# Kernel tuning notes

Measured on AMD Instinct MI355X. Metric: run time of the kernel, lower is better.

Reference implementation:

```python
import jax, jax.numpy as jnp
import numpy as np

LEAKY_ALPHA = 0.2
EPS_NORM = 1e-07


def _leaky_relu(x):
    return jnp.where(x >= 0, x, LEAKY_ALPHA * x)


def setup_inputs() -> dict:
    key = jax.random.key(0)
    ks = jax.random.split(key, 10)
    B, N, F = 16, 1024, 256
    H, Q, K, V = 4, 128, 128, 128
    return {
        "e": jax.random.normal(ks[0], (B, N, N), dtype=jnp.float32),
        "x_atm": jax.random.normal(ks[1], (B, N, F), dtype=jnp.float32),
        "mask": jnp.ones((B, N), dtype=jnp.float32),
        "eps": jax.random.normal(ks[2], (1,), dtype=jnp.float32) * 0.02,
        "Wq": jax.random.normal(ks[3], (H, F, Q), dtype=jnp.float32) * 0.05,
        "Wk": jax.random.normal(ks[4], (H, F, K), dtype=jnp.float32) * 0.05,
        "Wv": jax.random.normal(ks[5], (H, F, V), dtype=jnp.float32) * 0.05,
        "aq": jax.random.normal(ks[6], (H, Q), dtype=jnp.float32) * 0.05,
        "bq": jnp.zeros((H,), dtype=jnp.float32),
        "ak": jax.random.normal(ks[7], (H, K), dtype=jnp.float32) * 0.05,
        "bk": jnp.zeros((H,), dtype=jnp.float32),
    }


def reference(e, x_atm, mask, eps, Wq, Wk, Wv, aq, bq, ak, bk):
    B, N, _ = e.shape
    # add learned eps to the diagonal of e (set_diag(diag + eps))
    e_mod = e + eps[0] * jnp.eye(N, dtype=e.dtype)  # [B,N,N]

    # per-head query/key scalars: Dense -> LeakyReLU -> Dense(1)
    q = jnp.einsum("bhnq,hq->bhn", _leaky_relu(jnp.einsum("bnf,hfq->bhnq", x_atm, Wq)), aq) + bq[None, :, None]  # [B,H,N]
    k = jnp.einsum("bhnk,hk->bhn", _leaky_relu(jnp.einsum("bnf,hfk->bhnk", x_atm, Wk)), ak) + bk[None, :, None]  # [B,H,N]

    # attn[b,h,i,j] = tanh((q_i + k_j) * e_mod[b,i,j])
    scores = jnp.tanh((q[..., :, None] + k[..., None, :]) * e_mod[:, None, :, :])  # [B,H,N,N]

    # L2-normalize each row (tf.linalg.normalize norm + 1e-7)
    norm = jnp.sqrt(jnp.sum(scores * scores, axis=-1, keepdims=True)) + EPS_NORM
    attn = scores / norm

    # values and aggregation
    v = jnp.einsum("bnf,hfv->bhnv", x_atm, Wv)  # [B,H,N,V] (dropout rate 0 -> identity)
    out = jnp.einsum("bhij,bhjv->bhiv", attn, v)  # [B,H,N,V]

    # pooling == 'mask': sum over nodes weighted by mask -> [B,H,V]
    pooled = jnp.einsum("bhnv,bn->bhv", out, mask)

    # concat heads along feature axis -> [B, H*V]
    return pooled.reshape(B, -1)
```

## Files before the change

kernel.cpp:

```cpp
#include <hip/hip_runtime.h>

#define B_ 16
#define N_ 1024
#define F_ 256
#define H_ 4
#define QDIM 128

#define TANH_PRESCALE 2.8853900817779268f

typedef __attribute__((ext_vector_type(8))) short bf16x8;
typedef __attribute__((ext_vector_type(4))) float f32x4;
typedef __attribute__((ext_vector_type(2))) float f32x2;

__device__ __forceinline__ float leaky(float x) {
    return x >= 0.f ? x : 0.2f * x;
}

__device__ __forceinline__ unsigned short bfbits(float f) {
    unsigned u = __float_as_uint(f);
    return (unsigned short)((u + 0x7fffu + ((u >> 16) & 1u)) >> 16);
}

__device__ __forceinline__ float bf2f(unsigned short u) {
    return __uint_as_float(((unsigned)u) << 16);
}

__global__ __launch_bounds__(256) void convert_all(
    const float4* __restrict__ x4, ushort4* __restrict__ xh4,
    const float* __restrict__ Wq, const float* __restrict__ Wk,
    ushort* __restrict__ Wqt, ushort* __restrict__ Wkt)
{
    const int bx = blockIdx.x;
    if (bx < 2048) {
        const int t = bx * 256 + threadIdx.x;
        const float4 a = x4[2 * t], b = x4[2 * t + 1];
        ushort4 o0, o1;
        o0.x = bfbits(a.x); o0.y = bfbits(a.y); o0.z = bfbits(a.z); o0.w = bfbits(a.w);
        o1.x = bfbits(b.x); o1.y = bfbits(b.y); o1.z = bfbits(b.z); o1.w = bfbits(b.w);
        xh4[2 * t] = o0; xh4[2 * t + 1] = o1;
    } else {
        const int t2 = (bx - 2048) * 256 + threadIdx.x;
        const int z = t2 >> 17, t = t2 & 131071;
        const int f = t & 255, q = (t >> 8) & 127, h = t >> 15;
        const float* W = z ? Wk : Wq;
        ushort* O = z ? Wkt : Wqt;
        O[t] = bfbits(W[(h * 256 + f) * 128 + q]);
    }
}

__global__ __launch_bounds__(256) void qk_mfma(
    const ushort* __restrict__ xh,
    const ushort* __restrict__ Wqt, const ushort* __restrict__ Wkt,
    const float* __restrict__ aq, const float* __restrict__ bq,
    const float* __restrict__ ak, const float* __restrict__ bk,
    float* __restrict__ qbuf, float* __restrict__ kbuf)
{
    const int tid = threadIdx.x;
    const int mt  = blockIdx.x;
    const int h   = blockIdx.y;
    const bool isQ = (blockIdx.z == 0);
    const ushort* Wt = isQ ? Wqt : Wkt;
    const float*  av = isQ ? aq : ak;
    const float*  bv = isQ ? bq : bk;
    float* out = isQ ? qbuf : kbuf;

    __shared__ char  xs[64 * 512];
    __shared__ float sp[4][64];

    {
        const int r = tid >> 2;
        const uint4* src = reinterpret_cast<const uint4*>(xh + (size_t)(mt * 64 + r) * 256);
        #pragma unroll
        for (int i = 0; i < 8; ++i) {
            const int c = (tid & 3) + 4 * i;
            const uint4 v = src[c];
            *reinterpret_cast<uint4*>(xs + r * 512 + ((c ^ (r & 7)) << 4)) = v;
        }
    }
    __syncthreads();

    const int l  = tid & 63, w = tid >> 6;
    const int g  = l >> 4, li = l & 15;

    bf16x8 Bf[8][2];
    #pragma unroll
    for (int nf = 0; nf < 2; ++nf) {
        const int c = w * 32 + nf * 16 + li;
        const ushort* bp = Wt + ((size_t)(h * 128 + c)) * 256 + 8 * g;
        #pragma unroll
        for (int s = 0; s < 8; ++s)
            Bf[s][nf] = *reinterpret_cast<const bf16x8*>(bp + s * 32);
    }

    f32x4 acc[4][2];
    #pragma unroll
    for (int m = 0; m < 4; ++m)
        #pragma unroll
        for (int nf = 0; nf < 2; ++nf)
            acc[m][nf] = (f32x4){0.f, 0.f, 0.f, 0.f};

    #pragma unroll
    for (int s = 0; s < 8; ++s) {
        #pragma unroll
        for (int m = 0; m < 4; ++m) {
            const int r = m * 16 + li;
            const int chunk = (4 * s + g) ^ (r & 7);
            const bf16x8 af = *reinterpret_cast<const bf16x8*>(xs + r * 512 + chunk * 16);
            acc[m][0] = __builtin_amdgcn_mfma_f32_16x16x32_bf16(af, Bf[s][0], acc[m][0], 0, 0, 0);
            acc[m][1] = __builtin_amdgcn_mfma_f32_16x16x32_bf16(af, Bf[s][1], acc[m][1], 0, 0, 0);
        }
    }

    float part[4][4];
    #pragma unroll
    for (int m = 0; m < 4; ++m)
        #pragma unroll
        for (int j = 0; j < 4; ++j) part[m][j] = 0.f;

    #pragma unroll
    for (int nf = 0; nf < 2; ++nf) {
        const float a_ = av[h * QDIM + w * 32 + nf * 16 + li];
        #pragma unroll
        for (int m = 0; m < 4; ++m)
            #pragma unroll
            for (int j = 0; j < 4; ++j)
                part[m][j] = fmaf(a_, leaky(acc[m][nf][j]), part[m][j]);
    }
    #pragma unroll
    for (int mask = 1; mask < 16; mask <<= 1)
        #pragma unroll
        for (int m = 0; m < 4; ++m)
            #pragma unroll
            for (int j = 0; j < 4; ++j)
                part[m][j] += __shfl_xor(part[m][j], mask, 64);

    if (li == 0) {
        #pragma unroll
        for (int m = 0; m < 4; ++m)
            #pragma unroll
            for (int j = 0; j < 4; ++j)
                sp[w][m * 16 + g * 4 + j] = part[m][j];
    }
    __syncthreads();

    if (tid < 64) {
        const float val = (sp[0][tid] + sp[1][tid] + sp[2][tid] + sp[3][tid] + bv[h]) * TANH_PRESCALE;
        const int R = mt * 64 + tid;
        out[((R >> 10) * H_ + h) * N_ + (R & 1023)] = val;
    }
}

__global__ __launch_bounds__(512) void attn_kernel(
    const float* __restrict__ e,
    const float* __restrict__ qbuf, const float* __restrict__ kbuf,
    const float* __restrict__ mask, const float* __restrict__ epsp,
    ushort* __restrict__ pbuf)
{
    const int tid  = threadIdx.x;
    const int wav  = tid >> 6;
    const int h    = wav & 3;
    const int half = wav >> 2;
    const int lane = tid & 63;
    const int b    = blockIdx.y;
    const int ic   = blockIdx.x;
    const int i0   = ic * 16 + half * 8;
    const float epsv = epsp[0];
    const int udiag = ic >> 4;

    __shared__ f32x2 red2[4][8][64];

    const f32x4* kr4 = reinterpret_cast<const f32x4*>(kbuf + (b * H_ + h) * N_);
    f32x2 kk2[8];
    #pragma unroll
    for (int u = 0; u < 4; ++u) {
        const f32x4 kv = kr4[u * 64 + lane];
        kk2[2 * u]     = __builtin_shufflevector(kv, kv, 0, 1);
        kk2[2 * u + 1] = __builtin_shufflevector(kv, kv, 2, 3);
    }

    f32x2 wacc2[8];
    #pragma unroll
    for (int p = 0; p < 8; ++p) wacc2[p] = (f32x2){0.f, 0.f};

    const float* qrow  = qbuf + (b * H_ + h) * N_;
    const float* mrow  = mask + b * N_;
    const f32x4* ebase = reinterpret_cast<const f32x4*>(e + ((size_t)b << 20)) + lane;

    const f32x2 one2 = {1.f, 1.f};
    const f32x2 m2   = {-2.f, -2.f};

    #pragma unroll 2
    for (int ii = 0; ii < 8; ++ii) {
        const int i = i0 + ii;
        const float qi = qrow[i];
        const f32x2 qi2 = {qi, qi};
        const f32x4* er4 = ebase + ((size_t)i << 8);
        const bool isdl = (lane == ((i >> 2) & 63));
        const float dadd = isdl ? epsv : 0.f;
        f32x2 pv[8];
        f32x2 sslv = {0.f, 0.f};
        #pragma unroll
        for (int u = 0; u < 4; ++u) {
            const f32x4 ev = er4[u * 64];
            #pragma unroll
            for (int s = 0; s < 2; ++s) {
                const int p = 2 * u + s;
                const f32x2 ev2 = s ? __builtin_shufflevector(ev, ev, 2, 3)
                                    : __builtin_shufflevector(ev, ev, 0, 1);
                const f32x2 qk2 = qi2 + kk2[p];
                f32x2 arg2 = qk2 * ev2;
                if (u == udiag && s == ((ii & 3) >> 1)) {
                    const int cc = ii & 1;
                    arg2[cc] = fmaf(qk2[cc], dadd, arg2[cc]);
                }
                f32x2 ex;
                ex[0] = __builtin_amdgcn_exp2f(arg2[0]);
                ex[1] = __builtin_amdgcn_exp2f(arg2[1]);
                const f32x2 d2 = ex + one2;
                f32x2 r2;
                r2[0] = __builtin_amdgcn_rcpf(d2[0]);
                r2[1] = __builtin_amdgcn_rcpf(d2[1]);
                const f32x2 pvv = __builtin_elementwise_fma(r2, m2, one2);
                pv[p] = pvv;
                sslv = __builtin_elementwise_fma(pvv, pvv, sslv);
            }
        }
        float ssl = sslv[0] + sslv[1];
        #pragma unroll
        for (int m = 1; m < 64; m <<= 1) ssl += __shfl_xor(ssl, m, 64);
        const float scale = mrow[i] * __builtin_amdgcn_rcpf(sqrtf(ssl) + 1e-7f);
        const f32x2 sc2 = {scale, scale};
        #pragma unroll
        for (int p = 0; p < 8; ++p)
            wacc2[p] = __builtin_elementwise_fma(sc2, pv[p], wacc2[p]);
    }

    if (half == 1) {
        #pragma unroll
        for (int p = 0; p < 8; ++p) red2[h][p][lane] = wacc2[p];
    }
    __syncthreads();
    if (half == 0) {
        ushort* pr = pbuf + ((size_t)((ic * 16 + b) * H_ + h) << 10);
        #pragma unroll
        for (int u = 0; u < 4; ++u) {
            const f32x2 a = wacc2[2 * u]     + red2[h][2 * u][lane];
            const f32x2 c = wacc2[2 * u + 1] + red2[h][2 * u + 1][lane];
            ushort4 o;
            o.x = bfbits(a[0]); o.y = bfbits(a[1]);
            o.z = bfbits(c[0]); o.w = bfbits(c[1]);
            *reinterpret_cast<ushort4*>(pr + u * 256 + lane * 4) = o;
        }
    }
}

__global__ __launch_bounds__(256) void ypart_kernel(
    const ushort* __restrict__ xh, const ushort* __restrict__ pbuf,
    float* __restrict__ ypart)
{
    const int tid = threadIdx.x;
    const int bx  = blockIdx.x;
    const int b   = bx >> 4;
    const int jc  = bx & 15;
    const int j0  = jc * 64;

    __shared__ float ws_[H_][64];
    {
        const int hh = tid >> 6, j = tid & 63;
        const ushort* pp = pbuf + ((size_t)(b * H_ + hh) << 10) + j0 + j;
        float s0 = 0.f, s1 = 0.f, s2 = 0.f, s3 = 0.f;
        #pragma unroll 4
        for (int ic = 0; ic < 64; ic += 4) {
            s0 += bf2f(pp[(size_t)(ic + 0) * 65536]);
            s1 += bf2f(pp[(size_t)(ic + 1) * 65536]);
            s2 += bf2f(pp[(size_t)(ic + 2) * 65536]);
            s3 += bf2f(pp[(size_t)(ic + 3) * 65536]);
        }
        ws_[hh][j] = (s0 + s1) + (s2 + s3);
    }
    __syncthreads();

    float a0 = 0.f, a1 = 0.f, a2 = 0.f, a3 = 0.f;
    const ushort* xcol = xh + ((size_t)(b * N_ + j0)) * F_ + tid;
    #pragma unroll 4
    for (int j = 0; j < 64; ++j) {
        const float xv = bf2f(xcol[(size_t)j * F_]);
        a0 = fmaf(ws_[0][j], xv, a0);
        a1 = fmaf(ws_[1][j], xv, a1);
        a2 = fmaf(ws_[2][j], xv, a2);
        a3 = fmaf(ws_[3][j], xv, a3);
    }
    float* yp = ypart + (size_t)(b * 16 + jc) * (H_ * F_) + tid;
    yp[0 * F_] = a0; yp[1 * F_] = a1; yp[2 * F_] = a2; yp[3 * F_] = a3;
}

__global__ __launch_bounds__(256) void pool_kernel(
    const float* __restrict__ ypart, const float* __restrict__ Wv,
    float* __restrict__ out)
{
    const int tid = threadIdx.x;
    const int bh  = blockIdx.x;
    const int b   = bh >> 2;
    const int h   = bh & 3;
    __shared__ float ys[256];
    float s = 0.f;
    #pragma unroll
    for (int jc = 0; jc < 16; ++jc)
        s += ypart[(size_t)(b * 16 + jc) * (H_ * F_) + h * F_ + tid];
    ys[tid] = s;
    __syncthreads();
    if (tid < 128) {
        float acc = 0.f;
        const float* wv = Wv + h * (F_ * 128) + tid;
        #pragma unroll 4
        for (int f = 0; f < F_; ++f) acc = fmaf(ys[f], wv[f * 128], acc);
        out[bh * 128 + tid] = acc;
    }
}

extern "C" void kernel_launch(void* const* d_in, const int* in_sizes, int n_in,
                              void* d_out, int out_size, void* d_ws, size_t ws_size,
                              hipStream_t stream) {
    const float* e    = (const float*)d_in[0];
    const float* x    = (const float*)d_in[1];
    const float* mask = (const float*)d_in[2];
    const float* eps  = (const float*)d_in[3];
    const float* Wq   = (const float*)d_in[4];
    const float* Wk   = (const float*)d_in[5];
    const float* Wv   = (const float*)d_in[6];
    const float* aq   = (const float*)d_in[7];
    const float* bq   = (const float*)d_in[8];
    const float* ak   = (const float*)d_in[9];
    const float* bk   = (const float*)d_in[10];

    float*  qbuf  = (float*)d_ws;
    float*  kbuf  = qbuf + 65536;
    float*  ypartb= kbuf + 65536;
    ushort* pbuf  = (ushort*)(ypartb + 262144);
    ushort* xh    = pbuf + 4194304;
    ushort* Wqt   = xh + 4194304;
    ushort* Wkt   = Wqt + 131072;
    float*  outf  = (float*)d_out;

    convert_all<<<3072, 256, 0, stream>>>((const float4*)x, (ushort4*)xh, Wq, Wk, Wqt, Wkt);
    qk_mfma<<<dim3(256, 4, 2), 256, 0, stream>>>(xh, Wqt, Wkt, aq, bq, ak, bk, qbuf, kbuf);
    attn_kernel<<<dim3(64, 16), 512, 0, stream>>>(e, qbuf, kbuf, mask, eps, pbuf);
    ypart_kernel<<<256, 256, 0, stream>>>(xh, pbuf, ypartb);
    pool_kernel<<<64, 256, 0, stream>>>(ypartb, Wv, outf);
}
```

Measured before the change: 83.57 us.

## Fuse x bf16 conversion into qk GEMM, share x tile across heads, cheapen tanh

The standalone conversion of x to bf16 is removed. qk_mfma now loads fp32 x and converts it to bf16 while staging into shared memory. Each block then loops over two heads and both the Q and K projections, so the staged tile is reused four times. ypart reads fp32 x directly. In attn_kernel the two reciprocals per pair are replaced with one reciprocal of the product, with the argument clamped to 126 so the product cannot overflow. This removes one launch and the xh write and re-read, and halves rcp work in the hot loop. In exchange it adds a serial loop in qk_mfma, halves that grid, and makes ypart read fp32 instead of bf16.

```diff
diff --git a/kernel.cpp b/kernel.cpp
--- a/kernel.cpp
+++ b/kernel.cpp
@@ -25,31 +25,19 @@
     return __uint_as_float(((unsigned)u) << 16);
 }
 
-__global__ __launch_bounds__(256) void convert_all(
-    const float4* __restrict__ x4, ushort4* __restrict__ xh4,
+__global__ __launch_bounds__(256) void convert_w(
     const float* __restrict__ Wq, const float* __restrict__ Wk,
     ushort* __restrict__ Wqt, ushort* __restrict__ Wkt)
 {
-    const int bx = blockIdx.x;
-    if (bx < 2048) {
-        const int t = bx * 256 + threadIdx.x;
-        const float4 a = x4[2 * t], b = x4[2 * t + 1];
-        ushort4 o0, o1;
-        o0.x = bfbits(a.x); o0.y = bfbits(a.y); o0.z = bfbits(a.z); o0.w = bfbits(a.w);
-        o1.x = bfbits(b.x); o1.y = bfbits(b.y); o1.z = bfbits(b.z); o1.w = bfbits(b.w);
-        xh4[2 * t] = o0; xh4[2 * t + 1] = o1;
-    } else {
-        const int t2 = (bx - 2048) * 256 + threadIdx.x;
-        const int z = t2 >> 17, t = t2 & 131071;
-        const int f = t & 255, q = (t >> 8) & 127, h = t >> 15;
-        const float* W = z ? Wk : Wq;
-        ushort* O = z ? Wkt : Wqt;
-        O[t] = bfbits(W[(h * 256 + f) * 128 + q]);
-    }
+    const int t = blockIdx.x * 256 + threadIdx.x;
+    const int f = t & 255, q = (t >> 8) & 127, h = t >> 15;
+    const float* W = blockIdx.y ? Wk : Wq;
+    ushort* O = blockIdx.y ? Wkt : Wqt;
+    O[t] = bfbits(W[(h * 256 + f) * 128 + q]);
 }
 
 __global__ __launch_bounds__(256) void qk_mfma(
-    const ushort* __restrict__ xh,
+    const float* __restrict__ x,
     const ushort* __restrict__ Wqt, const ushort* __restrict__ Wkt,
     const float* __restrict__ aq, const float* __restrict__ bq,
     const float* __restrict__ ak, const float* __restrict__ bk,
@@ -57,24 +45,25 @@
 {
     const int tid = threadIdx.x;
     const int mt  = blockIdx.x;
-    const int h   = blockIdx.y;
-    const bool isQ = (blockIdx.z == 0);
-    const ushort* Wt = isQ ? Wqt : Wkt;
-    const float*  av = isQ ? aq : ak;
-    const float*  bv = isQ ? bq : bk;
-    float* out = isQ ? qbuf : kbuf;
+    const int hg  = blockIdx.y;
 
     __shared__ char  xs[64 * 512];
     __shared__ float sp[4][64];
 
     {
         const int r = tid >> 2;
-        const uint4* src = reinterpret_cast<const uint4*>(xh + (size_t)(mt * 64 + r) * 256);
+        const float* src = x + (size_t)(mt * 64 + r) * 256;
         #pragma unroll
         for (int i = 0; i < 8; ++i) {
             const int c = (tid & 3) + 4 * i;
-            const uint4 v = src[c];
-            *reinterpret_cast<uint4*>(xs + r * 512 + ((c ^ (r & 7)) << 4)) = v;
+            const float4 v0 = *reinterpret_cast<const float4*>(src + c * 8);
+            const float4 v1 = *reinterpret_cast<const float4*>(src + c * 8 + 4);
+            ushort4 o0, o1;
+            o0.x = bfbits(v0.x); o0.y = bfbits(v0.y); o0.z = bfbits(v0.z); o0.w = bfbits(v0.w);
+            o1.x = bfbits(v1.x); o1.y = bfbits(v1.y); o1.z = bfbits(v1.z); o1.w = bfbits(v1.w);
+            char* dst = xs + r * 512 + ((c ^ (r & 7)) << 4);
+            *reinterpret_cast<ushort4*>(dst) = o0;
+            *reinterpret_cast<ushort4*>(dst + 8) = o1;
         }
     }
     __syncthreads();
@@ -82,71 +71,82 @@
     const int l  = tid & 63, w = tid >> 6;
     const int g  = l >> 4, li = l & 15;
 
-    bf16x8 Bf[8][2];
-    #pragma unroll
-    for (int nf = 0; nf < 2; ++nf) {
-        const int c = w * 32 + nf * 16 + li;
-        const ushort* bp = Wt + ((size_t)(h * 128 + c)) * 256 + 8 * g;
-        #pragma unroll
-        for (int s = 0; s < 8; ++s)
-            Bf[s][nf] = *reinterpret_cast<const bf16x8*>(bp + s * 32);
-    }
-
-    f32x4 acc[4][2];
-    #pragma unroll
-    for (int m = 0; m < 4; ++m)
-        #pragma unroll
-        for (int nf = 0; nf < 2; ++nf)
-            acc[m][nf] = (f32x4){0.f, 0.f, 0.f, 0.f};
-
-    #pragma unroll
-    for (int s = 0; s < 8; ++s) {
-        #pragma unroll
-        for (int m = 0; m < 4; ++m) {
-            const int r = m * 16 + li;
-            const int chunk = (4 * s + g) ^ (r & 7);
-            const bf16x8 af = *reinterpret_cast<const bf16x8*>(xs + r * 512 + chunk * 16);
-            acc[m][0] = __builtin_amdgcn_mfma_f32_16x16x32_bf16(af, Bf[s][0], acc[m][0], 0, 0, 0);
-            acc[m][1] = __builtin_amdgcn_mfma_f32_16x16x32_bf16(af, Bf[s][1], acc[m][1], 0, 0, 0);
-        }
-    }
-
-    float part[4][4];
-    #pragma unroll
-    for (int m = 0; m < 4; ++m)
-        #pragma unroll
-        for (int j = 0; j < 4; ++j) part[m][j] = 0.f;
-
-    #pragma unroll
-    for (int nf = 0; nf < 2; ++nf) {
-        const float a_ = av[h * QDIM + w * 32 + nf * 16 + li];
+    #pragma unroll 1
+    for (int combo = 0; combo < 4; ++combo) {
+        const int h = hg * 2 + (combo >> 1);
+        const bool isQ = (combo & 1) == 0;
+        const ushort* Wt = isQ ? Wqt : Wkt;
+        const float*  av = isQ ? aq : ak;
+        const float*  bv = isQ ? bq : bk;
+        float* out = isQ ? qbuf : kbuf;
+
+        bf16x8 Bf[8][2];
+        #pragma unroll
+        for (int nf = 0; nf < 2; ++nf) {
+            const int c = w * 32 + nf * 16 + li;
+            const ushort* bp = Wt + ((size_t)(h * 128 + c)) * 256 + 8 * g;
+            #pragma unroll
+            for (int s = 0; s < 8; ++s)
+                Bf[s][nf] = *reinterpret_cast<const bf16x8*>(bp + s * 32);
+        }
+
+        f32x4 acc[4][2];
         #pragma unroll
         for (int m = 0; m < 4; ++m)
             #pragma unroll
-            for (int j = 0; j < 4; ++j)
-                part[m][j] = fmaf(a_, leaky(acc[m][nf][j]), part[m][j]);
-    }
-    #pragma unroll
-    for (int mask = 1; mask < 16; mask <<= 1)
+            for (int nf = 0; nf < 2; ++nf)
+                acc[m][nf] = (f32x4){0.f, 0.f, 0.f, 0.f};
+
+        #pragma unroll
+        for (int s = 0; s < 8; ++s) {
+            #pragma unroll
+            for (int m = 0; m < 4; ++m) {
+                const int r = m * 16 + li;
+                const int chunk = (4 * s + g) ^ (r & 7);
+                const bf16x8 af = *reinterpret_cast<const bf16x8*>(xs + r * 512 + chunk * 16);
+                acc[m][0] = __builtin_amdgcn_mfma_f32_16x16x32_bf16(af, Bf[s][0], acc[m][0], 0, 0, 0);
+                acc[m][1] = __builtin_amdgcn_mfma_f32_16x16x32_bf16(af, Bf[s][1], acc[m][1], 0, 0, 0);
+            }
+        }
+
+        float part[4][4];
         #pragma unroll
         for (int m = 0; m < 4; ++m)
             #pragma unroll
-            for (int j = 0; j < 4; ++j)
-                part[m][j] += __shfl_xor(part[m][j], mask, 64);
-
-    if (li == 0) {
-        #pragma unroll
-        for (int m = 0; m < 4; ++m)
-            #pragma unroll
-            for (int j = 0; j < 4; ++j)
-                sp[w][m * 16 + g * 4 + j] = part[m][j];
-    }
-    __syncthreads();
-
-    if (tid < 64) {
-        const float val = (sp[0][tid] + sp[1][tid] + sp[2][tid] + sp[3][tid] + bv[h]) * TANH_PRESCALE;
-        const int R = mt * 64 + tid;
-        out[((R >> 10) * H_ + h) * N_ + (R & 1023)] = val;
+            for (int j = 0; j < 4; ++j) part[m][j] = 0.f;
+
+        #pragma unroll
+        for (int nf = 0; nf < 2; ++nf) {
+            const float a_ = av[h * QDIM + w * 32 + nf * 16 + li];
+            #pragma unroll
+            for (int m = 0; m < 4; ++m)
+                #pragma unroll
+                for (int j = 0; j < 4; ++j)
+                    part[m][j] = fmaf(a_, leaky(acc[m][nf][j]), part[m][j]);
+        }
+        #pragma unroll
+        for (int mask = 1; mask < 16; mask <<= 1)
+            #pragma unroll
+            for (int m = 0; m < 4; ++m)
+                #pragma unroll
+                for (int j = 0; j < 4; ++j)
+                    part[m][j] += __shfl_xor(part[m][j], mask, 64);
+
+        if (li == 0) {
+            #pragma unroll
+            for (int m = 0; m < 4; ++m)
+                #pragma unroll
+                for (int j = 0; j < 4; ++j)
+                    sp[w][m * 16 + g * 4 + j] = part[m][j];
+        }
+        __syncthreads();
+
+        if (tid < 64) {
+            const float val = (sp[0][tid] + sp[1][tid] + sp[2][tid] + sp[3][tid] + bv[h]) * TANH_PRESCALE;
+            const int R = mt * 64 + tid;
+            out[((R >> 10) * H_ + h) * N_ + (R & 1023)] = val;
+        }
+        __syncthreads();
     }
 }
 
@@ -188,6 +188,7 @@
 
     const f32x2 one2 = {1.f, 1.f};
     const f32x2 m2   = {-2.f, -2.f};
+    const f32x2 c126 = {126.f, 126.f};
 
     #pragma unroll 2
     for (int ii = 0; ii < 8; ++ii) {
@@ -213,14 +214,15 @@
                     const int cc = ii & 1;
                     arg2[cc] = fmaf(qk2[cc], dadd, arg2[cc]);
                 }
+                arg2 = __builtin_elementwise_min(arg2, c126);
                 f32x2 ex;
                 ex[0] = __builtin_amdgcn_exp2f(arg2[0]);
                 ex[1] = __builtin_amdgcn_exp2f(arg2[1]);
                 const f32x2 d2 = ex + one2;
-                f32x2 r2;
-                r2[0] = __builtin_amdgcn_rcpf(d2[0]);
-                r2[1] = __builtin_amdgcn_rcpf(d2[1]);
-                const f32x2 pvv = __builtin_elementwise_fma(r2, m2, one2);
+                const float r1 = __builtin_amdgcn_rcpf(d2[0] * d2[1]);
+                const f32x2 d2s = __builtin_shufflevector(d2, d2, 1, 0);
+                const f32x2 rr2 = d2s * (f32x2){r1, r1};
+                const f32x2 pvv = __builtin_elementwise_fma(rr2, m2, one2);
                 pv[p] = pvv;
                 sslv = __builtin_elementwise_fma(pvv, pvv, sslv);
             }
@@ -255,7 +257,7 @@
 }
 
 __global__ __launch_bounds__(256) void ypart_kernel(
-    const ushort* __restrict__ xh, const ushort* __restrict__ pbuf,
+    const float* __restrict__ x, const ushort* __restrict__ pbuf,
     float* __restrict__ ypart)
 {
     const int tid = threadIdx.x;
@@ -281,10 +283,10 @@
     __syncthreads();
 
     float a0 = 0.f, a1 = 0.f, a2 = 0.f, a3 = 0.f;
-    const ushort* xcol = xh + ((size_t)(b * N_ + j0)) * F_ + tid;
+    const float* xcol = x + ((size_t)(b * N_ + j0)) * F_ + tid;
     #pragma unroll 4
     for (int j = 0; j < 64; ++j) {
-        const float xv = bf2f(xcol[(size_t)j * F_]);
+        const float xv = xcol[(size_t)j * F_];
         a0 = fmaf(ws_[0][j], xv, a0);
         a1 = fmaf(ws_[1][j], xv, a1);
         a2 = fmaf(ws_[2][j], xv, a2);
@@ -337,14 +339,13 @@
     float*  kbuf  = qbuf + 65536;
     float*  ypartb= kbuf + 65536;
     ushort* pbuf  = (ushort*)(ypartb + 262144);
-    ushort* xh    = pbuf + 4194304;
-    ushort* Wqt   = xh + 4194304;
+    ushort* Wqt   = pbuf + 4194304;
     ushort* Wkt   = Wqt + 131072;
     float*  outf  = (float*)d_out;
 
-    convert_all<<<3072, 256, 0, stream>>>((const float4*)x, (ushort4*)xh, Wq, Wk, Wqt, Wkt);
-    qk_mfma<<<dim3(256, 4, 2), 256, 0, stream>>>(xh, Wqt, Wkt, aq, bq, ak, bk, qbuf, kbuf);
+    convert_w<<<dim3(512, 2), 256, 0, stream>>>(Wq, Wk, Wqt, Wkt);
+    qk_mfma<<<dim3(256, 2), 256, 0, stream>>>(x, Wqt, Wkt, aq, bq, ak, bk, qbuf, kbuf);
     attn_kernel<<<dim3(64, 16), 512, 0, stream>>>(e, qbuf, kbuf, mask, eps, pbuf);
-    ypart_kernel<<<256, 256, 0, stream>>>(xh, pbuf, ypartb);
+    ypart_kernel<<<256, 256, 0, stream>>>(x, pbuf, ypartb);
     pool_kernel<<<64, 256, 0, stream>>>(ypartb, Wv, outf);
 }
```

Measured after the change: 89.19 us. +6.7%, slower.

## Double-buffer e rows in pairs and use DPP for wave reductions

Applied to the files above, without the earlier changes.

The 8-row loop is fully unrolled into pairs of rows, with register double-buffering so the loads of the next two e rows are issued before the current pair is computed. Two rows are processed together to interleave their transcendental ops, and the row sum-of-squares reduction uses DPP intra-row adds before the cross-row shuffles. The aim is to hide global-load latency and shorten the reduction. In exchange it uses more registers, which may lower occupancy.

```diff
diff --git a/kernel.cpp b/kernel.cpp
--- a/kernel.cpp
+++ b/kernel.cpp
@@ -23,6 +23,22 @@
 
 __device__ __forceinline__ float bf2f(unsigned short u) {
     return __uint_as_float(((unsigned)u) << 16);
+}
+
+template <int CTRL>
+__device__ __forceinline__ float dpp_add(float x) {
+    return x + __int_as_float(
+        __builtin_amdgcn_update_dpp(0, __float_as_int(x), CTRL, 0xf, 0xf, true));
+}
+
+__device__ __forceinline__ float wave_reduce_add(float x) {
+    x = dpp_add<0xB1>(x);
+    x = dpp_add<0x4E>(x);
+    x = dpp_add<0x141>(x);
+    x = dpp_add<0x140>(x);
+    x += __shfl_xor(x, 16, 64);
+    x += __shfl_xor(x, 32, 64);
+    return x;
 }
 
 __global__ __launch_bounds__(256) void convert_all(
@@ -189,51 +205,84 @@
     const f32x2 one2 = {1.f, 1.f};
     const f32x2 m2   = {-2.f, -2.f};
 
-    #pragma unroll 2
-    for (int ii = 0; ii < 8; ++ii) {
-        const int i = i0 + ii;
-        const float qi = qrow[i];
-        const f32x2 qi2 = {qi, qi};
-        const f32x4* er4 = ebase + ((size_t)i << 8);
-        const bool isdl = (lane == ((i >> 2) & 63));
-        const float dadd = isdl ? epsv : 0.f;
-        f32x2 pv[8];
-        f32x2 sslv = {0.f, 0.f};
-        #pragma unroll
-        for (int u = 0; u < 4; ++u) {
-            const f32x4 ev = er4[u * 64];
-            #pragma unroll
-            for (int s = 0; s < 2; ++s) {
-                const int p = 2 * u + s;
-                const f32x2 ev2 = s ? __builtin_shufflevector(ev, ev, 2, 3)
-                                    : __builtin_shufflevector(ev, ev, 0, 1);
-                const f32x2 qk2 = qi2 + kk2[p];
-                f32x2 arg2 = qk2 * ev2;
-                if (u == udiag && s == ((ii & 3) >> 1)) {
-                    const int cc = ii & 1;
-                    arg2[cc] = fmaf(qk2[cc], dadd, arg2[cc]);
-                }
-                f32x2 ex;
-                ex[0] = __builtin_amdgcn_exp2f(arg2[0]);
-                ex[1] = __builtin_amdgcn_exp2f(arg2[1]);
-                const f32x2 d2 = ex + one2;
-                f32x2 r2;
-                r2[0] = __builtin_amdgcn_rcpf(d2[0]);
-                r2[1] = __builtin_amdgcn_rcpf(d2[1]);
-                const f32x2 pvv = __builtin_elementwise_fma(r2, m2, one2);
-                pv[p] = pvv;
-                sslv = __builtin_elementwise_fma(pvv, pvv, sslv);
-            }
-        }
-        float ssl = sslv[0] + sslv[1];
-        #pragma unroll
-        for (int m = 1; m < 64; m <<= 1) ssl += __shfl_xor(ssl, m, 64);
-        const float scale = mrow[i] * __builtin_amdgcn_rcpf(sqrtf(ssl) + 1e-7f);
-        const f32x2 sc2 = {scale, scale};
-        #pragma unroll
-        for (int p = 0; p < 8; ++p)
-            wacc2[p] = __builtin_elementwise_fma(sc2, pv[p], wacc2[p]);
-    }
+    f32x4 bufA0[4], bufB0[4], bufA1[4], bufB1[4];
+
+#define LOADPAIR(IA, DA, DB)                                                   \
+    {                                                                          \
+        const f32x4* erA_ = ebase + ((size_t)(IA) << 8);                       \
+        const f32x4* erB_ = ebase + ((size_t)((IA) + 1) << 8);                 \
+        _Pragma("unroll")                                                      \
+        for (int u = 0; u < 4; ++u) { DA[u] = erA_[u * 64]; DB[u] = erB_[u * 64]; } \
+    }
+
+#define COMPUTE_PAIR(II, EA, EB)                                               \
+    {                                                                          \
+        const int iA = i0 + (II), iB = iA + 1;                                 \
+        const float qiA = qrow[iA], qiB = qrow[iB];                            \
+        const f32x2 qiA2 = {qiA, qiA}, qiB2 = {qiB, qiB};                      \
+        const bool isdl = (lane == ((iA >> 2) & 63));                          \
+        const float dadd = isdl ? epsv : 0.f;                                  \
+        f32x2 pvA[8], pvB[8];                                                  \
+        f32x2 sslA = {0.f, 0.f}, sslB = {0.f, 0.f};                            \
+        _Pragma("unroll")                                                      \
+        for (int u = 0; u < 4; ++u) {                                          \
+            _Pragma("unroll")                                                  \
+            for (int s = 0; s < 2; ++s) {                                      \
+                const int p = 2 * u + s;                                       \
+                const f32x2 eA2 = s ? __builtin_shufflevector(EA[u], EA[u], 2, 3) \
+                                    : __builtin_shufflevector(EA[u], EA[u], 0, 1); \
+                const f32x2 eB2 = s ? __builtin_shufflevector(EB[u], EB[u], 2, 3) \
+                                    : __builtin_shufflevector(EB[u], EB[u], 0, 1); \
+                const f32x2 qkA = qiA2 + kk2[p];                               \
+                const f32x2 qkB = qiB2 + kk2[p];                               \
+                f32x2 argA = qkA * eA2;                                        \
+                f32x2 argB = qkB * eB2;                                        \
+                if (u == udiag && s == (((II) & 3) >> 1)) {                    \
+                    argA[0] = fmaf(qkA[0], dadd, argA[0]);                     \
+                    argB[1] = fmaf(qkB[1], dadd, argB[1]);                     \
+                }                                                              \
+                f32x2 exA, exB;                                                \
+                exA[0] = __builtin_amdgcn_exp2f(argA[0]);                      \
+                exB[0] = __builtin_amdgcn_exp2f(argB[0]);                      \
+                exA[1] = __builtin_amdgcn_exp2f(argA[1]);                      \
+                exB[1] = __builtin_amdgcn_exp2f(argB[1]);                      \
+                const f32x2 dA = exA + one2;                                   \
+                const f32x2 dB = exB + one2;                                   \
+                f32x2 rA, rB;                                                  \
+                rA[0] = __builtin_amdgcn_rcpf(dA[0]);                          \
+                rB[0] = __builtin_amdgcn_rcpf(dB[0]);                          \
+                rA[1] = __builtin_amdgcn_rcpf(dA[1]);                          \
+                rB[1] = __builtin_amdgcn_rcpf(dB[1]);                          \
+                const f32x2 pA = __builtin_elementwise_fma(rA, m2, one2);      \
+                const f32x2 pB = __builtin_elementwise_fma(rB, m2, one2);      \
+                pvA[p] = pA; pvB[p] = pB;                                      \
+                sslA = __builtin_elementwise_fma(pA, pA, sslA);                \
+                sslB = __builtin_elementwise_fma(pB, pB, sslB);                \
+            }                                                                  \
+        }                                                                      \
+        const float sA = wave_reduce_add(sslA[0] + sslA[1]);                   \
+        const float sB = wave_reduce_add(sslB[0] + sslB[1]);                   \
+        const float scaleA = mrow[iA] * __builtin_amdgcn_rcpf(sqrtf(sA) + 1e-7f); \
+        const float scaleB = mrow[iB] * __builtin_amdgcn_rcpf(sqrtf(sB) + 1e-7f); \
+        const f32x2 scA = {scaleA, scaleA}, scB = {scaleB, scaleB};            \
+        _Pragma("unroll")                                                      \
+        for (int p = 0; p < 8; ++p) {                                          \
+            wacc2[p] = __builtin_elementwise_fma(scA, pvA[p], wacc2[p]);       \
+            wacc2[p] = __builtin_elementwise_fma(scB, pvB[p], wacc2[p]);       \
+        }                                                                      \
+    }
+
+    LOADPAIR(i0 + 0, bufA0, bufB0);
+    LOADPAIR(i0 + 2, bufA1, bufB1);
+    COMPUTE_PAIR(0, bufA0, bufB0);
+    LOADPAIR(i0 + 4, bufA0, bufB0);
+    COMPUTE_PAIR(2, bufA1, bufB1);
+    LOADPAIR(i0 + 6, bufA1, bufB1);
+    COMPUTE_PAIR(4, bufA0, bufB0);
+    COMPUTE_PAIR(6, bufA1, bufB1);
+
+#undef LOADPAIR
+#undef COMPUTE_PAIR
 
     if (half == 1) {
         #pragma unroll
```

Result: faster. 80.23 us (-4.0%).
